# Optimization experiments

Hardware: AMD Instinct MI355X
Metric: run time of the kernel (lower is better)

Reference implementation:

```python
import jax, jax.numpy as jnp
import numpy as np

B, S, H = 2, 2048, 2048
NH, NKV, HD = 32, 8, 64
GROUPS = NH // NKV
SCALE = HD ** -0.5


def _rope_tables(key):
    # Real RoPE cos/sin tables (HF Llama style), shape [B, S, HD]
    inv_freq = 1.0 / (10000.0 ** (jnp.arange(0, HD, 2, dtype=jnp.float32) / HD))  # [HD/2]
    t = jnp.arange(S, dtype=jnp.float32)
    freqs = jnp.outer(t, inv_freq)                      # [S, HD/2]
    emb = jnp.concatenate([freqs, freqs], axis=-1)      # [S, HD]
    cos = jnp.broadcast_to(jnp.cos(emb)[None], (B, S, HD))
    sin = jnp.broadcast_to(jnp.sin(emb)[None], (B, S, HD))
    return cos, sin


def setup_inputs() -> dict:
    key = jax.random.key(0)
    ks = jax.random.split(key, 9)
    w = 0.02
    cos, sin = _rope_tables(key)
    return {
        "hidden_states": jax.random.normal(ks[0], (B, S, H), jnp.float32),
        "bounding_box_embeddings": jax.random.normal(ks[1], (B, S, H), jnp.float32),
        "cos": cos,
        "sin": sin,
        "Wq": jax.random.normal(ks[2], (H, NH * HD), jnp.float32) * w,
        "Wk": jax.random.normal(ks[3], (H, NKV * HD), jnp.float32) * w,
        "Wv": jax.random.normal(ks[4], (H, NKV * HD), jnp.float32) * w,
        "Wo": jax.random.normal(ks[5], (NH * HD, H), jnp.float32) * w,
        "Wsq": jax.random.normal(ks[6], (H, NH * HD), jnp.float32) * w,
        "Wsk": jax.random.normal(ks[7], (H, NKV * HD), jnp.float32) * w,
    }


def _rotate_half(x):
    x1, x2 = x[..., : HD // 2], x[..., HD // 2 :]
    return jnp.concatenate([-x2, x1], axis=-1)


def _apply_rope(q, k, cos, sin):
    # q: [B,NH,S,HD], k: [B,NKV,S,HD]; cos/sin [B,S,HD] -> broadcast over heads
    c = cos[:, None, :, :]
    s = sin[:, None, :, :]
    return q * c + _rotate_half(q) * s, k * c + _rotate_half(k) * s


def _proj_heads(x, W, n_heads):
    b, s, _ = x.shape
    return (x @ W).reshape(b, s, n_heads, HD).transpose(0, 2, 1, 3)  # [B,nh,S,HD]


def reference(hidden_states, bounding_box_embeddings, cos, sin, Wq, Wk, Wv, Wo, Wsq, Wsk):
    # Text Q/K/V with RoPE
    q = _proj_heads(hidden_states, Wq, NH)
    k = _proj_heads(hidden_states, Wk, NKV)
    v = _proj_heads(hidden_states, Wv, NKV)
    q, k = _apply_rope(q, k, cos, sin)
    # Spatial Q/K (no V) with RoPE
    sq = _proj_heads(bounding_box_embeddings, Wsq, NH)
    sk = _proj_heads(bounding_box_embeddings, Wsk, NKV)
    sq, sk = _apply_rope(sq, sk, cos, sin)
    # Fused text+spatial states, then GQA repeat_kv
    q = q + sq                                   # [B,NH,S,HD]
    k = jnp.repeat(k + sk, GROUPS, axis=1)       # [B,NH,S,HD]
    v = jnp.repeat(v, GROUPS, axis=1)            # [B,NH,S,HD]
    # Eager attention with causal mask
    scores = jnp.einsum("bhqd,bhkd->bhqk", q, k) * SCALE
    causal = jnp.tril(jnp.ones((S, S), dtype=bool))
    scores = jnp.where(causal[None, None], scores, jnp.finfo(jnp.float32).min)
    probs = jax.nn.softmax(scores.astype(jnp.float32), axis=-1).astype(q.dtype)
    attn = jnp.einsum("bhqk,bhkd->bhqd", probs, v)           # [B,NH,S,HD]
    attn = attn.transpose(0, 2, 1, 3).reshape(B, S, NH * HD)  # [B,S,NH*HD]
    return attn @ Wo
```

## Files before the change

### kernel.cpp

```cpp
#include <hip/hip_runtime.h>

#define B_ 2
#define S_ 2048
#define H_ 2048
#define NH_ 32
#define NKV_ 8
#define HD_ 64

typedef short short8 __attribute__((ext_vector_type(8)));
typedef float f32x4 __attribute__((ext_vector_type(4)));
typedef float f32x16 __attribute__((ext_vector_type(16)));
typedef unsigned int uint4v __attribute__((ext_vector_type(4)));

__device__ __forceinline__ float bf2f(unsigned short u) {
  union { unsigned int i; float f; } v; v.i = ((unsigned int)u) << 16; return v.f;
}
__device__ __forceinline__ unsigned short f2bf(float f) {
  union { float f; unsigned int i; } v; v.f = f;
  unsigned int u = v.i;
  u += 0x7fffu + ((u >> 16) & 1u);
  return (unsigned short)(u >> 16);
}
__device__ __forceinline__ unsigned int cvtpk(float lo, float hi) {
  unsigned int r;
  asm("v_cvt_pk_bf16_f32 %0, %1, %2" : "=v"(r) : "v"(lo), "v"(hi));
  return r;
}
__device__ __forceinline__ void pl32swap(unsigned int& a, unsigned int& b) {
  asm("v_permlane32_swap_b32 %0, %1" : "+v"(a), "+v"(b));
}
__device__ __forceinline__ short8 mkfrag(unsigned a, unsigned b, unsigned c, unsigned d) {
  union { uint4v u; short8 s; } x;
  x.u = (uint4v){a, b, c, d};
  return x.s;
}
__device__ __forceinline__ void gload_lds16(const unsigned short* g, unsigned short* l) {
  __builtin_amdgcn_global_load_lds((const __attribute__((address_space(1))) void*)g,
                                   (__attribute__((address_space(3))) void*)l,
                                   16, 0, 0);
}
#define MFMA32(A, B, C) __builtin_amdgcn_mfma_f32_32x32x16_bf16(A, B, C, 0, 0, 0)

__global__ __launch_bounds__(256) void cast_f32_bf16(const float* __restrict__ in,
                                                     unsigned short* __restrict__ out,
                                                     int n8) {
  int i = blockIdx.x * 256 + threadIdx.x;
  if (i >= n8) return;
  float4 v0 = ((const float4*)in)[i * 2];
  float4 v1 = ((const float4*)in)[i * 2 + 1];
  ushort4 o0, o1;
  o0.x = f2bf(v0.x); o0.y = f2bf(v0.y); o0.z = f2bf(v0.z); o0.w = f2bf(v0.w);
  o1.x = f2bf(v1.x); o1.y = f2bf(v1.y); o1.z = f2bf(v1.z); o1.w = f2bf(v1.w);
  ((ushort4*)out)[i * 2] = o0;
  ((ushort4*)out)[i * 2 + 1] = o1;
}

__global__ __launch_bounds__(256) void transpose_cast(const float* __restrict__ W,
                                                      unsigned short* __restrict__ Wt,
                                                      int N, int K) {
  __shared__ float tile[32][33];
  int n0 = blockIdx.x * 32, k0 = blockIdx.y * 32;
  int tx = threadIdx.x & 31;
  int ty = threadIdx.x >> 5;
#pragma unroll
  for (int i = 0; i < 32; i += 8)
    tile[ty + i][tx] = W[(size_t)(k0 + ty + i) * N + n0 + tx];
  __syncthreads();
#pragma unroll
  for (int i = 0; i < 32; i += 8)
    Wt[(size_t)(n0 + ty + i) * K + k0 + tx] = f2bf(tile[tx][ty + i]);
}

__global__ __launch_bounds__(256) void vtrans_kernel(const unsigned short* __restrict__ P1,
                                                     unsigned short* __restrict__ Vt) {
  __shared__ unsigned short tile[32][33];
  int s0 = blockIdx.x * 32, d0 = blockIdx.y * 32, bk = blockIdx.z;
  int b = bk >> 3, kv = bk & 7;
  int tx = threadIdx.x & 31, ty = threadIdx.x >> 5;
#pragma unroll
  for (int i = 0; i < 32; i += 8)
    tile[ty + i][tx] = P1[(size_t)(b * S_ + s0 + ty + i) * 3072 + 2560 + kv * 64 + d0 + tx];
  __syncthreads();
#pragma unroll
  for (int i = 0; i < 32; i += 8)
    Vt[(size_t)(bk * 64 + d0 + ty + i) * S_ + s0 + tx] = tile[tx][ty + i];
}

__global__ __launch_bounds__(256) void combine_rope(const unsigned short* __restrict__ P1,
                                                    const unsigned short* __restrict__ P2,
                                                    const float* __restrict__ cosT,
                                                    const float* __restrict__ sinT,
                                                    unsigned short* __restrict__ Qb,
                                                    unsigned short* __restrict__ Kb) {
  int id = blockIdx.x * 256 + threadIdx.x;
  int row = id / 640;
  int grp = id - row * 640;
  int b = row >> 11;
  int s = row & 2047;
  bool isQ = grp < 512;
  int n = isQ ? grp * 4 : (grp - 512) * 4;
  int h = n >> 6;
  int d = n & 63;
  int base = isQ ? 0 : 2048;
  const int ld1 = 3072, ld2 = 2560;
  int pd = (d < 32) ? d + 32 : d - 32;
  float sign = (d < 32) ? -1.f : 1.f;
  int pcol = base + h * 64 + pd;

  ushort4 a1 = *(const ushort4*)&P1[(size_t)row * ld1 + base + n];
  ushort4 a2 = *(const ushort4*)&P2[(size_t)row * ld2 + base + n];
  ushort4 b1 = *(const ushort4*)&P1[(size_t)row * ld1 + pcol];
  ushort4 b2 = *(const ushort4*)&P2[(size_t)row * ld2 + pcol];
  float4 cv = *(const float4*)&cosT[(size_t)row * 64 + d];
  float4 sv = *(const float4*)&sinT[(size_t)row * 64 + d];
  float scale = isQ ? 0.125f : 1.0f;

  float xs[4] = { bf2f(a1.x) + bf2f(a2.x), bf2f(a1.y) + bf2f(a2.y),
                  bf2f(a1.z) + bf2f(a2.z), bf2f(a1.w) + bf2f(a2.w) };
  float xp[4] = { bf2f(b1.x) + bf2f(b2.x), bf2f(b1.y) + bf2f(b2.y),
                  bf2f(b1.z) + bf2f(b2.z), bf2f(b1.w) + bf2f(b2.w) };
  float cc[4] = { cv.x, cv.y, cv.z, cv.w };
  float ss[4] = { sv.x, sv.y, sv.z, sv.w };
  ushort4 o;
  unsigned short* op = (unsigned short*)&o;
#pragma unroll
  for (int i = 0; i < 4; ++i)
    op[i] = f2bf((xs[i] * cc[i] + sign * xp[i] * ss[i]) * scale);

  if (isQ)
    *(ushort4*)&Qb[((size_t)(b * NH_ + h) * S_ + s) * HD_ + d] = o;
  else
    *(ushort4*)&Kb[((size_t)(b * NKV_ + h) * S_ + s) * HD_ + d] = o;
}

template <int OF32>
__global__ __launch_bounds__(256) void gemm_bt(const unsigned short* __restrict__ A,
                                               const unsigned short* __restrict__ Bt,
                                               void* __restrict__ Cv,
                                               int N, int K, int nbx) {
  __shared__ unsigned short lA[128 * 32];
  __shared__ unsigned short lB[128 * 32];
  int nwg = gridDim.x;
  int orig = blockIdx.x;
  int wgid = (orig & 7) * (nwg >> 3) + (orig >> 3);
  int bn = wgid % nbx;
  int bm = wgid / nbx;
  int t = threadIdx.x;
  int w = t >> 6, l = t & 63, g = l >> 4, c = l & 15;
  int wr = w >> 1, wc = w & 1;

  int srow = w * 16 + (l >> 2);
  int scol = (l & 3) * 8;
  const unsigned short* gA0 = A + (size_t)(bm * 128 + srow) * K + scol;
  const unsigned short* gA1 = A + (size_t)(bm * 128 + 64 + srow) * K + scol;
  const unsigned short* gB0 = Bt + (size_t)(bn * 128 + srow) * K + scol;
  const unsigned short* gB1 = Bt + (size_t)(bn * 128 + 64 + srow) * K + scol;
  unsigned short* lA0 = &lA[w * 512];
  unsigned short* lA1 = &lA[2048 + w * 512];
  unsigned short* lB0 = &lB[w * 512];
  unsigned short* lB1 = &lB[2048 + w * 512];

  f32x4 acc[4][4];
#pragma unroll
  for (int m = 0; m < 4; ++m)
#pragma unroll
    for (int n = 0; n < 4; ++n) acc[m][n] = 0.f;

  for (int k0 = 0; k0 < K; k0 += 32) {
    __syncthreads();
    gload_lds16(gA0 + k0, lA0);
    gload_lds16(gA1 + k0, lA1);
    gload_lds16(gB0 + k0, lB0);
    gload_lds16(gB1 + k0, lB1);
    __syncthreads();

    short8 a[4], bfr[4];
#pragma unroll
    for (int m = 0; m < 4; ++m)
      a[m] = *(const short8*)&lA[(wr * 64 + m * 16 + c) * 32 + g * 8];
#pragma unroll
    for (int n = 0; n < 4; ++n)
      bfr[n] = *(const short8*)&lB[(wc * 64 + n * 16 + c) * 32 + g * 8];
#pragma unroll
    for (int m = 0; m < 4; ++m)
#pragma unroll
      for (int n = 0; n < 4; ++n)
        acc[m][n] = __builtin_amdgcn_mfma_f32_16x16x32_bf16(a[m], bfr[n], acc[m][n], 0, 0, 0);
  }

#pragma unroll
  for (int m = 0; m < 4; ++m) {
#pragma unroll
    for (int n = 0; n < 4; ++n) {
#pragma unroll
      for (int r = 0; r < 4; ++r) {
        int row = bm * 128 + wr * 64 + m * 16 + g * 4 + r;
        int col = bn * 128 + wc * 64 + n * 16 + c;
        if constexpr (OF32)
          ((float*)Cv)[(size_t)row * N + col] = acc[m][n][r];
        else
          ((unsigned short*)Cv)[(size_t)row * N + col] = f2bf(acc[m][n][r]);
      }
    }
  }
}

__global__ __launch_bounds__(512) void attn_kernel(const unsigned short* __restrict__ Q,
                                                   const unsigned short* __restrict__ K,
                                                   const unsigned short* __restrict__ Vt,
                                                   unsigned short* __restrict__ attnOut) {
  __shared__ unsigned short lK[2][64 * 64];
  __shared__ unsigned short lV[2][64 * 64];

  int bx = blockIdx.x;
  int j = bx & 7;
  int bh = bx >> 3;
  int head = bh & 31;
  int b = bh >> 5;
  int kvh = head >> 2;
  const unsigned short* Kp = K + (size_t)(b * NKV_ + kvh) * S_ * HD_;
  const unsigned short* Vp = Vt + (size_t)(b * NKV_ + kvh) * HD_ * S_;

  int t = threadIdx.x;
  int w = t >> 6, l = t & 63;
  int q32 = l & 31, hf = l >> 5;
  int qb_eff = (w < 4) ? j : (15 - j);
  int qbase_w = qb_eff * 128 + (w & 3) * 32;
  const unsigned short* Qp = Q + ((size_t)(b * NH_ + head) * S_ + qbase_w) * HD_;

  short8 qf[4];
  {
    const unsigned short* qrow = Qp + (size_t)q32 * HD_ + hf * 8;
#pragma unroll
    for (int kc = 0; kc < 4; ++kc)
      qf[kc] = *(const short8*)(qrow + kc * 16);
  }

  int srow = t >> 3;
  int sslot = t & 7;
  unsigned lOff = srow * 128 + ((sslot ^ (srow & 7)) << 4);
  const char* gK0 = (const char*)(Kp + (size_t)srow * 64 + sslot * 8);
  const char* gV0 = (const char*)(Vp + (size_t)srow * 2048 + sslot * 8);

  {
    int4 rk = *(const int4*)(gK0);
    int4 rv = *(const int4*)(gV0);
    *(int4*)((char*)lK[0] + lOff) = rk;
    *(int4*)((char*)lV[0] + lOff) = rv;
  }
  __syncthreads();

  f32x16 oA = 0.f, oB = 0.f;
  float mrun = -1e30f, lrun = 0.f;

  int nt = 32 - 2 * j;
  int cur = 0;
  for (int tI = 0; tI < nt; ++tI) {
    int kv0 = tI * 64;
    bool pf = (tI + 1 < nt);
    int4 nk, nv;
    if (pf) {
      nk = *(const int4*)(gK0 + (size_t)(kv0 + 64) * 128);
      nv = *(const int4*)(gV0 + (size_t)(kv0 + 64) * 2);
    }

    if (kv0 <= qbase_w + 31) {
      const char* lKc = (const char*)lK[cur];
      const char* lVc = (const char*)lV[cur];
      int swz = q32 & 7;

      f32x16 sA = 0.f, sB = 0.f;
      __builtin_amdgcn_s_setprio(1);
#pragma unroll
      for (int kc = 0; kc < 4; ++kc) {
        int cs = (kc << 1) | hf;
        short8 ak0 = *(const short8*)(lKc + q32 * 128 + ((cs ^ swz) << 4));
        short8 ak1 = *(const short8*)(lKc + (32 + q32) * 128 + ((cs ^ swz) << 4));
        sA = MFMA32(ak0, qf[kc], sA);
        sB = MFMA32(ak1, qf[kc], sB);
      }
      __builtin_amdgcn_s_setprio(0);

      if (kv0 + 63 > qbase_w) {
        int qg = qbase_w + q32;
#pragma unroll
        for (int r = 0; r < 16; ++r) {
          int kvr = kv0 + (r & 3) + ((r >> 2) << 3) + (hf << 2);
          if (kvr > qg) sA[r] = -1e30f;
          if (kvr + 32 > qg) sB[r] = -1e30f;
        }
      }

      float pmax = sA[0];
#pragma unroll
      for (int r = 1; r < 16; ++r) pmax = fmaxf(pmax, sA[r]);
#pragma unroll
      for (int r = 0; r < 16; ++r) pmax = fmaxf(pmax, sB[r]);
      pmax = fmaxf(pmax, __shfl_xor(pmax, 32, 64));

      if (!__all(pmax <= mrun + 8.f)) {
        float mnew = fmaxf(mrun, pmax);
        float sf = __expf(mrun - mnew);
        lrun *= sf;
        mrun = mnew;
#pragma unroll
        for (int r = 0; r < 16; ++r) {
          int src = (r & 3) + ((r >> 2) << 3) + (hf << 2);
          float sfr = __shfl(sf, src, 64);
          oA[r] *= sfr;
          oB[r] *= sfr;
        }
      }

      float rs = 0.f;
#pragma unroll
      for (int r = 0; r < 16; ++r) { sA[r] = __expf(sA[r] - mrun); rs += sA[r]; }
#pragma unroll
      for (int r = 0; r < 16; ++r) { sB[r] = __expf(sB[r] - mrun); rs += sB[r]; }
      rs += __shfl_xor(rs, 32, 64);
      lrun += rs;

      short8 paf[4];
      {
        unsigned c0 = cvtpk(sA[0], sA[1]), c1 = cvtpk(sA[2], sA[3]);
        unsigned c2 = cvtpk(sA[4], sA[5]), c3 = cvtpk(sA[6], sA[7]);
        pl32swap(c0, c2); pl32swap(c1, c3);
        paf[0] = mkfrag(c0, c1, c2, c3);
      }
      {
        unsigned c0 = cvtpk(sA[8], sA[9]),  c1 = cvtpk(sA[10], sA[11]);
        unsigned c2 = cvtpk(sA[12], sA[13]), c3 = cvtpk(sA[14], sA[15]);
        pl32swap(c0, c2); pl32swap(c1, c3);
        paf[1] = mkfrag(c0, c1, c2, c3);
      }
      {
        unsigned c0 = cvtpk(sB[0], sB[1]), c1 = cvtpk(sB[2], sB[3]);
        unsigned c2 = cvtpk(sB[4], sB[5]), c3 = cvtpk(sB[6], sB[7]);
        pl32swap(c0, c2); pl32swap(c1, c3);
        paf[2] = mkfrag(c0, c1, c2, c3);
      }
      {
        unsigned c0 = cvtpk(sB[8], sB[9]),  c1 = cvtpk(sB[10], sB[11]);
        unsigned c2 = cvtpk(sB[12], sB[13]), c3 = cvtpk(sB[14], sB[15]);
        pl32swap(c0, c2); pl32swap(c1, c3);
        paf[3] = mkfrag(c0, c1, c2, c3);
      }

      __builtin_amdgcn_s_setprio(1);
#pragma unroll
      for (int ks = 0; ks < 4; ++ks) {
        int cs = (ks << 1) | hf;
        short8 v0 = *(const short8*)(lVc + q32 * 128 + ((cs ^ swz) << 4));
        short8 v1 = *(const short8*)(lVc + (32 + q32) * 128 + ((cs ^ swz) << 4));
        oA = MFMA32(paf[ks], v0, oA);
        oB = MFMA32(paf[ks], v1, oB);
      }
      __builtin_amdgcn_s_setprio(0);
    }

    if (pf) {
      *(int4*)((char*)lK[cur ^ 1] + lOff) = nk;
      *(int4*)((char*)lV[cur ^ 1] + lOff) = nv;
    }
    __syncthreads();
    cur ^= 1;
  }

  float linv = 1.f / lrun;
#pragma unroll
  for (int r = 0; r < 16; ++r) {
    int src = (r & 3) + ((r >> 2) << 3) + (hf << 2);
    float li = __shfl(linv, src, 64);
    unsigned short* op = attnOut + ((size_t)(b * S_ + qbase_w + src)) * (NH_ * HD_) + head * 64;
    op[q32] = f2bf(oA[r] * li);
    op[32 + q32] = f2bf(oB[r] * li);
  }
}

extern "C" void kernel_launch(void* const* d_in, const int* in_sizes, int n_in,
                              void* d_out, int out_size, void* d_ws, size_t ws_size,
                              hipStream_t stream) {
  const float* hidden = (const float*)d_in[0];
  const float* bbox   = (const float*)d_in[1];
  const float* cosT   = (const float*)d_in[2];
  const float* sinT   = (const float*)d_in[3];
  const float* Wq  = (const float*)d_in[4];
  const float* Wk  = (const float*)d_in[5];
  const float* Wv  = (const float*)d_in[6];
  const float* Wo  = (const float*)d_in[7];
  const float* Wsq = (const float*)d_in[8];
  const float* Wsk = (const float*)d_in[9];

  char* ws = (char*)d_ws;
  size_t off = 0;
  auto alloc = [&](size_t bytes) {
    void* p = ws + off;
    off += (bytes + 255) & ~(size_t)255;
    return p;
  };
  unsigned short* WhT = (unsigned short*)alloc((size_t)3072 * 2048 * 2);
  unsigned short* WbT = (unsigned short*)alloc((size_t)2560 * 2048 * 2);
  unsigned short* WoT = (unsigned short*)alloc((size_t)2048 * 2048 * 2);
  unsigned short* P1  = (unsigned short*)alloc((size_t)4096 * 3072 * 2);
  unsigned short* P2  = (unsigned short*)alloc((size_t)4096 * 2560 * 2);
  unsigned short* Xh  = (unsigned short*)alloc((size_t)4096 * 2048 * 2);
  unsigned short* Xb  = (unsigned short*)alloc((size_t)4096 * 2048 * 2);
  unsigned short* attn = Xh;
  unsigned short* Qb   = Xb;
  unsigned short* Kb   = Xb + (size_t)B_ * NH_ * S_ * HD_;
  unsigned short* Vt   = Kb + (size_t)B_ * NKV_ * S_ * HD_;

  dim3 blk(256);
  cast_f32_bf16<<<dim3(4096), blk, 0, stream>>>(hidden, Xh, 4096 * 2048 / 8);
  cast_f32_bf16<<<dim3(4096), blk, 0, stream>>>(bbox,   Xb, 4096 * 2048 / 8);

  transpose_cast<<<dim3(64, 64), blk, 0, stream>>>(Wq,  WhT, 2048, 2048);
  transpose_cast<<<dim3(16, 64), blk, 0, stream>>>(Wk,  WhT + (size_t)2048 * 2048, 512, 2048);
  transpose_cast<<<dim3(16, 64), blk, 0, stream>>>(Wv,  WhT + (size_t)2560 * 2048, 512, 2048);
  transpose_cast<<<dim3(64, 64), blk, 0, stream>>>(Wsq, WbT, 2048, 2048);
  transpose_cast<<<dim3(16, 64), blk, 0, stream>>>(Wsk, WbT + (size_t)2048 * 2048, 512, 2048);
  transpose_cast<<<dim3(64, 64), blk, 0, stream>>>(Wo,  WoT, 2048, 2048);

  gemm_bt<0><<<dim3(32 * 24), blk, 0, stream>>>(Xh, WhT, P1, 3072, 2048, 24);
  gemm_bt<0><<<dim3(32 * 20), blk, 0, stream>>>(Xb, WbT, P2, 2560, 2048, 20);

  combine_rope<<<dim3((B_ * S_ * 640) / 256), blk, 0, stream>>>(P1, P2, cosT, sinT, Qb, Kb);
  vtrans_kernel<<<dim3(64, 2, 16), blk, 0, stream>>>(P1, Vt);

  attn_kernel<<<dim3(512), dim3(512), 0, stream>>>(Qb, Kb, Vt, attn);

  gemm_bt<1><<<dim3(32 * 16), blk, 0, stream>>>(attn, WoT, d_out, 2048, 2048, 16);
}
```

Baseline: 305.2 us.

## Replace 128x128 GEMM with double-buffered 256x256 tile, 8-wave pipelined kernel

Replaces the simple single-buffered 128x128 bf16 GEMM with a 256x256-tile, 512-thread kernel. It double-buffers LDS with 64-wide K steps and interleaves direct-to-LDS global loads of future tiles with MFMA phases, using explicit barriers, waitcnt and setprio. The aim is better operand reuse per tile and overlap of memory latency with matrix math across all three projection GEMMs. In exchange it launches fewer workgroups (128-192 on a large-CU GPU, so under-filled), uses 128KB of LDS, and hardcodes K=2048, with fragile hand scheduling.

```diff
diff --git a/kernel.cpp b/kernel.cpp
--- a/kernel.cpp
+++ b/kernel.cpp
@@ -133,73 +133,131 @@
     *(ushort4*)&Kb[((size_t)(b * NKV_ + h) * S_ + s) * HD_ + d] = o;
 }
 
+
+#define PHASE_FENCE() do { \
+  __builtin_amdgcn_s_barrier(); \
+  asm volatile("s_waitcnt lgkmcnt(0)" ::: "memory"); \
+  __builtin_amdgcn_sched_barrier(0); \
+} while (0)
+
+#define RD_A(BC, MH) do { \
+  _Pragma("unroll") for (int mf = 0; mf < 4; ++mf) { \
+    _Pragma("unroll") for (int ks = 0; ks < 2; ++ks) \
+      a[mf][ks] = *(const short8*)&lds[BC][((wm * 2 + (MH)) * 8 + mf * 2 + ks) * 512 + l * 8]; \
+  } \
+} while (0)
+
+#define RD_B(BC, NH, DST) do { \
+  _Pragma("unroll") for (int nf = 0; nf < 2; ++nf) { \
+    _Pragma("unroll") for (int ks = 0; ks < 2; ++ks) \
+      DST[nf][ks] = *(const short8*)&lds[BC][16384 + (((wn * 2 + (NH)) * 2 + nf) * 2 + ks) * 512 + l * 8]; \
+  } \
+} while (0)
+
+#define MM(MH, NH, BB) do { \
+  _Pragma("unroll") for (int mf = 0; mf < 4; ++mf) { \
+    _Pragma("unroll") for (int nf = 0; nf < 2; ++nf) { \
+      _Pragma("unroll") for (int ks = 0; ks < 2; ++ks) \
+        acc[(MH) * 4 + mf][(NH) * 2 + nf] = __builtin_amdgcn_mfma_f32_16x16x32_bf16( \
+            a[mf][ks], BB[nf][ks], acc[(MH) * 4 + mf][(NH) * 2 + nf], 0, 0, 0); \
+    } \
+  } \
+} while (0)
+
+#define STAGE_A(H, KT) do { \
+  int bq_ = (KT) & 1; \
+  gload_lds16(srcA0 + (size_t)(H) * (64 * 2048) + (KT) * 64, &lds[bq_][((H) * 8 + w) * 512]); \
+  gload_lds16(srcA1 + (size_t)(H) * (64 * 2048) + (KT) * 64, &lds[bq_][(16 + (H) * 8 + w) * 512]); \
+} while (0)
+
+#define STAGE_B(H, KT) do { \
+  int bq_ = (KT) & 1; \
+  gload_lds16(srcB0 + (size_t)(H) * (32 * 2048) + (KT) * 64, \
+              &lds[bq_][16384 + ((w >> 2) * 8 + (H) * 4 + (w & 3)) * 512]); \
+  gload_lds16(srcB1 + (size_t)(H) * (32 * 2048) + (KT) * 64, \
+              &lds[bq_][16384 + (16 + (w >> 2) * 8 + (H) * 4 + (w & 3)) * 512]); \
+} while (0)
+
+#define GROUP(BC, G) do { \
+  int kt1 = (G) + 1; if (kt1 > 31) kt1 = 31; \
+  int kt2 = (G) + 2; if (kt2 > 31) kt2 = 31; \
+   \
+  RD_A(BC, 0); RD_B(BC, 0, b0); \
+  STAGE_A(1, kt1); \
+  PHASE_FENCE(); \
+  __builtin_amdgcn_s_setprio(1); MM(0, 0, b0); __builtin_amdgcn_s_setprio(0); \
+  __builtin_amdgcn_s_barrier(); \
+   \
+  RD_B(BC, 1, b1); \
+  STAGE_A(0, kt2); \
+  PHASE_FENCE(); \
+  __builtin_amdgcn_s_setprio(1); MM(0, 1, b1); __builtin_amdgcn_s_setprio(0); \
+  __builtin_amdgcn_s_barrier(); \
+   \
+  RD_A(BC, 1); \
+  STAGE_B(0, kt2); \
+  PHASE_FENCE(); \
+  __builtin_amdgcn_s_setprio(1); MM(1, 0, b0); __builtin_amdgcn_s_setprio(0); \
+  __builtin_amdgcn_s_barrier(); \
+   \
+  STAGE_B(1, kt2); \
+  PHASE_FENCE(); \
+  __builtin_amdgcn_s_setprio(1); MM(1, 1, b1); __builtin_amdgcn_s_setprio(0); \
+  asm volatile("s_waitcnt vmcnt(6)" ::: "memory"); \
+  __builtin_amdgcn_s_barrier(); \
+} while (0)
+
 template <int OF32>
-__global__ __launch_bounds__(256) void gemm_bt(const unsigned short* __restrict__ A,
-                                               const unsigned short* __restrict__ Bt,
-                                               void* __restrict__ Cv,
-                                               int N, int K, int nbx) {
-  __shared__ unsigned short lA[128 * 32];
-  __shared__ unsigned short lB[128 * 32];
+__global__ __launch_bounds__(512, 2) void gemm256(const unsigned short* __restrict__ A,
+                                                  const unsigned short* __restrict__ Bt,
+                                                  void* __restrict__ Cv,
+                                                  int N, int nbx) {
+  __shared__ unsigned short lds[2][32768];
   int nwg = gridDim.x;
   int orig = blockIdx.x;
   int wgid = (orig & 7) * (nwg >> 3) + (orig >> 3);
-  int bn = wgid % nbx;
-  int bm = wgid / nbx;
-  int t = threadIdx.x;
-  int w = t >> 6, l = t & 63, g = l >> 4, c = l & 15;
-  int wr = w >> 1, wc = w & 1;
-
-  int srow = w * 16 + (l >> 2);
-  int scol = (l & 3) * 8;
-  const unsigned short* gA0 = A + (size_t)(bm * 128 + srow) * K + scol;
-  const unsigned short* gA1 = A + (size_t)(bm * 128 + 64 + srow) * K + scol;
-  const unsigned short* gB0 = Bt + (size_t)(bn * 128 + srow) * K + scol;
-  const unsigned short* gB1 = Bt + (size_t)(bn * 128 + 64 + srow) * K + scol;
-  unsigned short* lA0 = &lA[w * 512];
-  unsigned short* lA1 = &lA[2048 + w * 512];
-  unsigned short* lB0 = &lB[w * 512];
-  unsigned short* lB1 = &lB[2048 + w * 512];
-
-  f32x4 acc[4][4];
-#pragma unroll
-  for (int m = 0; m < 4; ++m)
-#pragma unroll
-    for (int n = 0; n < 4; ++n) acc[m][n] = 0.f;
-
-  for (int k0 = 0; k0 < K; k0 += 32) {
-    __syncthreads();
-    gload_lds16(gA0 + k0, lA0);
-    gload_lds16(gA1 + k0, lA1);
-    gload_lds16(gB0 + k0, lB0);
-    gload_lds16(gB1 + k0, lB1);
-    __syncthreads();
-
-    short8 a[4], bfr[4];
-#pragma unroll
-    for (int m = 0; m < 4; ++m)
-      a[m] = *(const short8*)&lA[(wr * 64 + m * 16 + c) * 32 + g * 8];
-#pragma unroll
-    for (int n = 0; n < 4; ++n)
-      bfr[n] = *(const short8*)&lB[(wc * 64 + n * 16 + c) * 32 + g * 8];
-#pragma unroll
-    for (int m = 0; m < 4; ++m)
-#pragma unroll
-      for (int n = 0; n < 4; ++n)
-        acc[m][n] = __builtin_amdgcn_mfma_f32_16x16x32_bf16(a[m], bfr[n], acc[m][n], 0, 0, 0);
-  }
-
-#pragma unroll
-  for (int m = 0; m < 4; ++m) {
-#pragma unroll
-    for (int n = 0; n < 4; ++n) {
+  int bn = wgid % nbx, bm = wgid / nbx;
+  int t = threadIdx.x, w = t >> 6, l = t & 63;
+  int wm = w >> 2, wn = w & 3;
+
+  int kcol = (w & 1) * 32 + ((t >> 4) & 3) * 8;
+  int rA0 = bm * 256 + ((w >> 1) & 3) * 16 + (t & 15);
+  const unsigned short* srcA0 = A + (size_t)rA0 * 2048 + kcol;
+  const unsigned short* srcA1 = srcA0 + (size_t)128 * 2048;
+  int nB0 = bn * 256 + (w >> 2) * 64 + ((w >> 1) & 1) * 16 + (t & 15);
+  const unsigned short* srcB0 = Bt + (size_t)nB0 * 2048 + kcol;
+  const unsigned short* srcB1 = srcB0 + (size_t)128 * 2048;
+
+  short8 a[4][2], b0[2][2], b1[2][2];
+  f32x4 acc[8][4];
+#pragma unroll
+  for (int mi = 0; mi < 8; ++mi)
+#pragma unroll
+    for (int ni = 0; ni < 4; ++ni) acc[mi][ni] = 0.f;
+
+  STAGE_A(0, 0); STAGE_B(0, 0); STAGE_B(1, 0); STAGE_A(1, 0);
+  STAGE_A(0, 1); STAGE_B(0, 1); STAGE_B(1, 1);
+  asm volatile("s_waitcnt vmcnt(6)" ::: "memory");
+  __builtin_amdgcn_s_barrier();
+
+  for (int tg = 0; tg < 32; tg += 2) {
+    GROUP(0, tg);
+    GROUP(1, tg + 1);
+  }
+  asm volatile("s_waitcnt vmcnt(0)" ::: "memory");
+
+#pragma unroll
+  for (int mi = 0; mi < 8; ++mi) {
+    int row = bm * 256 + wm * 128 + (mi >> 2) * 64 + (mi & 3) * 16 + (l >> 4) * 4;
+#pragma unroll
+    for (int ni = 0; ni < 4; ++ni) {
+      int col = bn * 256 + wn * 64 + (ni >> 1) * 32 + (ni & 1) * 16 + (l & 15);
 #pragma unroll
       for (int r = 0; r < 4; ++r) {
-        int row = bm * 128 + wr * 64 + m * 16 + g * 4 + r;
-        int col = bn * 128 + wc * 64 + n * 16 + c;
         if constexpr (OF32)
-          ((float*)Cv)[(size_t)row * N + col] = acc[m][n][r];
+          ((float*)Cv)[(size_t)(row + r) * N + col] = acc[mi][ni][r];
         else
-          ((unsigned short*)Cv)[(size_t)row * N + col] = f2bf(acc[m][n][r]);
+          ((unsigned short*)Cv)[(size_t)(row + r) * N + col] = f2bf(acc[mi][ni][r]);
       }
     }
   }
@@ -421,13 +479,13 @@
   transpose_cast<<<dim3(16, 64), blk, 0, stream>>>(Wsk, WbT + (size_t)2048 * 2048, 512, 2048);
   transpose_cast<<<dim3(64, 64), blk, 0, stream>>>(Wo,  WoT, 2048, 2048);
 
-  gemm_bt<0><<<dim3(32 * 24), blk, 0, stream>>>(Xh, WhT, P1, 3072, 2048, 24);
-  gemm_bt<0><<<dim3(32 * 20), blk, 0, stream>>>(Xb, WbT, P2, 2560, 2048, 20);
+  gemm256<0><<<dim3(192), dim3(512), 0, stream>>>(Xh, WhT, P1, 3072, 12);
+  gemm256<0><<<dim3(160), dim3(512), 0, stream>>>(Xb, WbT, P2, 2560, 10);
 
   combine_rope<<<dim3((B_ * S_ * 640) / 256), blk, 0, stream>>>(P1, P2, cosT, sinT, Qb, Kb);
   vtrans_kernel<<<dim3(64, 2, 16), blk, 0, stream>>>(P1, Vt);
 
   attn_kernel<<<dim3(512), dim3(512), 0, stream>>>(Qb, Kb, Vt, attn);
 
-  gemm_bt<1><<<dim3(32 * 16), blk, 0, stream>>>(attn, WoT, d_out, 2048, 2048, 16);
-}
+  gemm256<1><<<dim3(128), dim3(512), 0, stream>>>(attn, WoT, d_out, 2048, 8);
+}
```

Result: slower. 319.0 us (+4.5%).
